# Kernel tuning notes

Hardware: AMD Instinct MI355X
Metric: run time of the kernel (lower is better)

Reference implementation:

```python
import jax, jax.numpy as jnp
import numpy as np

SEQ_LEN = 512
JOINT_DIM = 96
DECAY = 0.8


def _predefined_weights(n: int, decay: float) -> np.ndarray:
    # W[i, j] = decay**(i-j) for j <= i, each row normalized to sum 1.
    i = np.arange(n)[:, None]
    j = np.arange(n)[None, :]
    lower = j <= i
    exponent = np.where(lower, i - j, 0)
    w = np.where(lower, decay ** exponent.astype(np.float64), 0.0)
    row_sum = w.sum(axis=1, keepdims=True)
    w = np.where(row_sum > 0, w / row_sum, w)
    return w.astype(np.float32)


def setup_inputs() -> dict:
    key = jax.random.key(0)
    kx, ko = jax.random.split(key)
    x = jax.random.normal(kx, (64, SEQ_LEN, JOINT_DIM), dtype=jnp.float32)
    # learnable parameter (initialized to zeros in the module; small noise for generality)
    learnable_offset = 0.02 * jax.random.normal(ko, (JOINT_DIM, SEQ_LEN, SEQ_LEN), dtype=jnp.float32)
    predefined_weights = jnp.asarray(_predefined_weights(SEQ_LEN, DECAY))
    return {"x": x, "learnable_offset": learnable_offset, "predefined_weights": predefined_weights}


def reference(x, learnable_offset, predefined_weights):
    # masks[j] = softmax(predefined + offset[j], axis=-1)   -> [J, N, N]
    masks = jax.nn.softmax(predefined_weights[None, :, :] + learnable_offset, axis=-1)
    # out[b, n, j] = sum_m masks[j, n, m] * x[b, m, j]      -> [B, N, J]
    return jnp.einsum('jnm,bmj->bnj', masks, x)
```

## Files before the change

kernel.cpp:

```cpp
#include <hip/hip_runtime.h>

#define BATCH 64
#define SEQ   512
#define JDIM  96
#define TN    64
#define KC    64
#define NCH   (SEQ / KC)
#define LDB   72

typedef __attribute__((ext_vector_type(8))) short bf16x8;
typedef __attribute__((ext_vector_type(4))) float f32x4;

#define LOG2D (-0.32192809489f)

__device__ __forceinline__ unsigned short f2bf(float f) {
  unsigned u = __float_as_uint(f);
  u += 0x7FFFu + ((u >> 16) & 1u);
  return (unsigned short)(u >> 16);
}

__global__ __launch_bounds__(256) void transpose_in_kernel(
    const float* __restrict__ x, unsigned short* __restrict__ xT) {
  __shared__ float tile[JDIM * 65];
  const int r0 = blockIdx.x * 64;
  const int R = BATCH * SEQ;
  for (int idx = threadIdx.x; idx < 64 * 24; idx += 256) {
    int rr = idx / 24, jg = idx - rr * 24;
    float4 v = *(const float4*)(x + (size_t)(r0 + rr) * JDIM + 4 * jg);
    tile[(4 * jg + 0) * 65 + rr] = v.x;
    tile[(4 * jg + 1) * 65 + rr] = v.y;
    tile[(4 * jg + 2) * 65 + rr] = v.z;
    tile[(4 * jg + 3) * 65 + rr] = v.w;
  }
  __syncthreads();
  for (int idx = threadIdx.x; idx < JDIM * 8; idx += 256) {
    int jj = idx >> 3, rg = idx & 7;
    const float* t = &tile[jj * 65 + 8 * rg];
    uint4 pk;
    pk.x = (unsigned)f2bf(t[0]) | ((unsigned)f2bf(t[1]) << 16);
    pk.y = (unsigned)f2bf(t[2]) | ((unsigned)f2bf(t[3]) << 16);
    pk.z = (unsigned)f2bf(t[4]) | ((unsigned)f2bf(t[5]) << 16);
    pk.w = (unsigned)f2bf(t[6]) | ((unsigned)f2bf(t[7]) << 16);
    *(uint4*)(&xT[(size_t)jj * R + r0 + 8 * rg]) = pk;
  }
}

__global__ __launch_bounds__(256, 3) void fused_kernel(
    const unsigned short* __restrict__ xT,
    const float* __restrict__ off,
    float* __restrict__ outT) {
  __shared__ unsigned short As[BATCH * LDB];
  __shared__ unsigned short Bs[TN * LDB];
  __shared__ float Lred[TN * 17];
  __shared__ float Linv[TN];

  const int j  = blockIdx.x >> 3;
  const int n0 = (blockIdx.x & 7) * TN;

  const int tid  = threadIdx.x;
  const int lane = tid & 63;
  const int wid  = tid >> 6;
  const int ln   = lane & 15;
  const int quad = lane >> 4;
  const int bw   = (wid & 1) * 32;
  const int nw   = (wid >> 1) * 32;

  f32x4 acc[2][2];
#pragma unroll
  for (int i = 0; i < 2; ++i)
#pragma unroll
    for (int q = 0; q < 2; ++q) acc[i][q] = (f32x4){0.f, 0.f, 0.f, 0.f};
  float Lpart[4] = {0.f, 0.f, 0.f, 0.f};

  const unsigned short* xTj = xT + (size_t)j * (BATCH * SEQ);
  const float* offj = off + (size_t)j * (SEQ * SEQ);

  const int a_kg = tid & 7;
  const int a_b  = tid >> 3;
  const int b_mg = tid & 15;
  const int b_n  = tid >> 4;

  float cn[4];
#pragma unroll
  for (int p = 0; p < 4; ++p) {
    const int n = n0 + b_n + 16 * p;
    cn[p] = 0.2f / (1.0f - exp2f(LOG2D * (float)(n + 1)));
  }

  for (int ch = 0; ch < NCH; ++ch) {
    const int m0 = ch * KC;
#pragma unroll
    for (int p = 0; p < 2; ++p) {
      const int b = a_b + 32 * p;
      uint4 v = *(const uint4*)(xTj + (size_t)b * SEQ + m0 + 8 * a_kg);
      *(uint4*)(&As[b * LDB + 8 * a_kg]) = v;
    }
    const int mbase = m0 + 4 * b_mg;
#pragma unroll
    for (int p = 0; p < 4; ++p) {
      const int nl = b_n + 16 * p;
      const int n  = n0 + nl;
      const float4 o = *(const float4*)(offj + (size_t)n * SEQ + mbase);
      const float c = cn[p];
      const float d0 = (float)(n - mbase);
      const float p0 = (d0 >= 0.f) ? c * exp2f(LOG2D * d0) : 0.f;
      const float p1 = (d0 >= 1.f) ? c * exp2f(LOG2D * (d0 - 1.f)) : 0.f;
      const float p2 = (d0 >= 2.f) ? c * exp2f(LOG2D * (d0 - 2.f)) : 0.f;
      const float p3 = (d0 >= 3.f) ? c * exp2f(LOG2D * (d0 - 3.f)) : 0.f;
      const float e0 = __expf(o.x + p0);
      const float e1 = __expf(o.y + p1);
      const float e2 = __expf(o.z + p2);
      const float e3 = __expf(o.w + p3);
      Lpart[p] += (e0 + e1) + (e2 + e3);
      uint2 pk;
      pk.x = (unsigned)f2bf(e0) | ((unsigned)f2bf(e1) << 16);
      pk.y = (unsigned)f2bf(e2) | ((unsigned)f2bf(e3) << 16);
      *(uint2*)(&Bs[nl * LDB + 4 * b_mg]) = pk;
    }
    __syncthreads();
#pragma unroll
    for (int ks = 0; ks < KC; ks += 32) {
      bf16x8 afrag[2], bfrag[2];
#pragma unroll
      for (int i = 0; i < 2; ++i)
        afrag[i] = *(const bf16x8*)(&As[(bw + 16 * i + ln) * LDB + ks + 8 * quad]);
#pragma unroll
      for (int q = 0; q < 2; ++q)
        bfrag[q] = *(const bf16x8*)(&Bs[(nw + 16 * q + ln) * LDB + ks + 8 * quad]);
#pragma unroll
      for (int i = 0; i < 2; ++i)
#pragma unroll
        for (int q = 0; q < 2; ++q)
          acc[i][q] = __builtin_amdgcn_mfma_f32_16x16x32_bf16(afrag[i], bfrag[q], acc[i][q], 0, 0, 0);
    }
    __syncthreads();
  }

#pragma unroll
  for (int p = 0; p < 4; ++p) Lred[(b_n + 16 * p) * 17 + b_mg] = Lpart[p];
  __syncthreads();
  if (tid < TN) {
    float s = 0.f;
#pragma unroll
    for (int i = 0; i < 16; ++i) s += Lred[tid * 17 + i];
    Linv[tid] = 1.0f / s;
  }
  __syncthreads();

  float* outTj = outT + (size_t)j * (SEQ * BATCH);
#pragma unroll
  for (int q = 0; q < 2; ++q) {
    const int nc = nw + 16 * q + ln;
    const float linv = Linv[nc];
#pragma unroll
    for (int i = 0; i < 2; ++i) {
      float4 v;
      v.x = acc[i][q][0] * linv;
      v.y = acc[i][q][1] * linv;
      v.z = acc[i][q][2] * linv;
      v.w = acc[i][q][3] * linv;
      *(float4*)(&outTj[(size_t)(n0 + nc) * BATCH + bw + 16 * i + 4 * quad]) = v;
    }
  }
}

__global__ __launch_bounds__(256) void transpose_out_kernel(
    const float* __restrict__ outT, float* __restrict__ out) {
  __shared__ float tile[JDIM * 65];
  const int n = blockIdx.x;
  for (int idx = threadIdx.x; idx < JDIM * 16; idx += 256) {
    int jj = idx >> 4, g = idx & 15;
    float4 v = *(const float4*)(outT + ((size_t)jj * SEQ + n) * BATCH + 4 * g);
    float* t = &tile[jj * 65 + 4 * g];
    t[0] = v.x; t[1] = v.y; t[2] = v.z; t[3] = v.w;
  }
  __syncthreads();
  for (int idx = threadIdx.x; idx < BATCH * 24; idx += 256) {
    int b = idx / 24, jg = idx - b * 24;
    float4 w;
    w.x = tile[(4 * jg + 0) * 65 + b];
    w.y = tile[(4 * jg + 1) * 65 + b];
    w.z = tile[(4 * jg + 2) * 65 + b];
    w.w = tile[(4 * jg + 3) * 65 + b];
    *(float4*)(out + ((size_t)b * SEQ + n) * JDIM + 4 * jg) = w;
  }
}

extern "C" void kernel_launch(void* const* d_in, const int* in_sizes, int n_in,
                              void* d_out, int out_size, void* d_ws, size_t ws_size,
                              hipStream_t stream) {
  const float* x   = (const float*)d_in[0];
  const float* off = (const float*)d_in[1];
  float* out = (float*)d_out;

  unsigned short* xT = (unsigned short*)d_ws;
  float* outT = (float*)((char*)d_ws + (size_t)JDIM * BATCH * SEQ * sizeof(unsigned short));

  transpose_in_kernel<<<BATCH * SEQ / 64, 256, 0, stream>>>(x, xT);
  fused_kernel<<<JDIM * (SEQ / TN), 256, 0, stream>>>(xT, off, outT);
  transpose_out_kernel<<<SEQ, 256, 0, stream>>>(outT, out);
}
```

Measured before the change: 173.7 us.

## Double-buffer fused kernel loads with async global-to-LDS DMA and swizzled layout

Replaces the register-staged global loads of xT and the offset tile with global_load_lds DMA into double-buffered, XOR-swizzled LDS buffers, so the next chunk is prefetched while the current one is processed. The exp computation is reorganised so each thread handles 16 consecutive columns of one row, using a running product (×1.25) instead of per-element exp2, and the bf16 B tile reuses the raw offset buffer in place. This aims to hide global memory latency and cut transcendental work, at the cost of more LDS, extra barriers with manual lgkmcnt waits, and a risk of lower occupancy.

```diff
diff --git a/kernel.cpp b/kernel.cpp
--- a/kernel.cpp
+++ b/kernel.cpp
@@ -7,17 +7,28 @@
 #define KC    64
 #define NCH   (SEQ / KC)
 #define LDB   72
+#define LOG2D (-0.32192809489f)
 
 typedef __attribute__((ext_vector_type(8))) short bf16x8;
 typedef __attribute__((ext_vector_type(4))) float f32x4;
-
-#define LOG2D (-0.32192809489f)
 
 __device__ __forceinline__ unsigned short f2bf(float f) {
   unsigned u = __float_as_uint(f);
   u += 0x7FFFu + ((u >> 16) & 1u);
   return (unsigned short)(u >> 16);
 }
+
+__device__ __forceinline__ void dma16(void* lds, const void* g) {
+  __builtin_amdgcn_global_load_lds(
+      (const __attribute__((address_space(1))) unsigned*)g,
+      (__attribute__((address_space(3))) unsigned*)lds, 16, 0, 0);
+}
+
+#define LGKM_BARRIER() do {                                  \
+  asm volatile("s_waitcnt lgkmcnt(0)" ::: "memory");         \
+  __builtin_amdgcn_s_barrier();                              \
+  asm volatile("" ::: "memory");                             \
+} while (0)
 
 __global__ __launch_bounds__(256) void transpose_in_kernel(
     const float* __restrict__ x, unsigned short* __restrict__ xT) {
@@ -49,9 +60,8 @@
     const unsigned short* __restrict__ xT,
     const float* __restrict__ off,
     float* __restrict__ outT) {
-  __shared__ unsigned short As[BATCH * LDB];
-  __shared__ unsigned short Bs[TN * LDB];
-  __shared__ float Lred[TN * 17];
+  __shared__ __align__(16) unsigned short Araw[2][BATCH * KC];
+  __shared__ __align__(16) float Oraw[2][TN * KC];
   __shared__ float Linv[TN];
 
   const int j  = blockIdx.x >> 3;
@@ -65,84 +75,130 @@
   const int bw   = (wid & 1) * 32;
   const int nw   = (wid >> 1) * 32;
 
-  f32x4 acc[2][2];
-#pragma unroll
-  for (int i = 0; i < 2; ++i)
-#pragma unroll
-    for (int q = 0; q < 2; ++q) acc[i][q] = (f32x4){0.f, 0.f, 0.f, 0.f};
-  float Lpart[4] = {0.f, 0.f, 0.f, 0.f};
-
   const unsigned short* xTj = xT + (size_t)j * (BATCH * SEQ);
   const float* offj = off + (size_t)j * (SEQ * SEQ);
 
-  const int a_kg = tid & 7;
-  const int a_b  = tid >> 3;
-  const int b_mg = tid & 15;
-  const int b_n  = tid >> 4;
-
-  float cn[4];
-#pragma unroll
-  for (int p = 0; p < 4; ++p) {
-    const int n = n0 + b_n + 16 * p;
-    cn[p] = 0.2f / (1.0f - exp2f(LOG2D * (float)(n + 1)));
-  }
+  const unsigned short* pA[2];
+  int aoff[2];
+#pragma unroll
+  for (int t = 0; t < 2; ++t) {
+    const int r = 8 * (2 * wid + t) + (lane >> 3);
+    const int g = (lane & 7) ^ (r & 7);
+    pA[t] = xTj + (size_t)r * SEQ + 8 * g;
+    aoff[t] = (2 * wid + t) * 1024;
+  }
+  const float* pO[4];
+  int ooff[4];
+#pragma unroll
+  for (int t = 0; t < 4; ++t) {
+    const int r = 4 * (4 * wid + t) + (lane >> 4);
+    const int g = (lane & 15) ^ (r & 15);
+    pO[t] = offj + (size_t)(n0 + r) * SEQ + 4 * g;
+    ooff[t] = (4 * wid + t) * 1024;
+  }
+
+#pragma unroll
+  for (int t = 0; t < 2; ++t) dma16((char*)&Araw[0][0] + aoff[t], pA[t]);
+#pragma unroll
+  for (int t = 0; t < 4; ++t) dma16((char*)&Oraw[0][0] + ooff[t], pO[t]);
+
+  f32x4 acc[2][2];
+#pragma unroll
+  for (int i = 0; i < 2; ++i)
+#pragma unroll
+    for (int q = 0; q < 2; ++q) acc[i][q] = (f32x4){0.f, 0.f, 0.f, 0.f};
+
+  const int nl  = tid >> 2;
+  const int sub = tid & 3;
+  const int nglob = n0 + nl;
+  const float cn = 0.2f / (1.0f - exp2f(LOG2D * (float)(nglob + 1)));
+  float Lpart = 0.f;
 
   for (int ch = 0; ch < NCH; ++ch) {
+    const int c = ch & 1;
+    __syncthreads();
+
+    if (ch + 1 < NCH) {
+#pragma unroll
+      for (int t = 0; t < 2; ++t) { pA[t] += KC; dma16((char*)&Araw[c ^ 1][0] + aoff[t], pA[t]); }
+#pragma unroll
+      for (int t = 0; t < 4; ++t) { pO[t] += KC; dma16((char*)&Oraw[c ^ 1][0] + ooff[t], pO[t]); }
+    }
+
+    const char* Ob = (const char*)&Oraw[c][0];
+    float4 o4[4];
+#pragma unroll
+    for (int e = 0; e < 4; ++e) {
+      const int gs = (4 * sub + e) ^ (nl & 15);
+      o4[e] = *(const float4*)(Ob + nl * 256 + gs * 16);
+    }
+    bf16x8 af[2][2];
+#pragma unroll
+    for (int ksI = 0; ksI < 2; ++ksI)
+#pragma unroll
+      for (int i = 0; i < 2; ++i) {
+        const int row = bw + 16 * i + ln;
+        const int gs = ((ksI << 2) + quad) ^ (ln & 7);
+        af[ksI][i] = *(const bf16x8*)((const char*)&Araw[c][0] + row * 128 + gs * 16);
+      }
     const int m0 = ch * KC;
-#pragma unroll
-    for (int p = 0; p < 2; ++p) {
-      const int b = a_b + 32 * p;
-      uint4 v = *(const uint4*)(xTj + (size_t)b * SEQ + m0 + 8 * a_kg);
-      *(uint4*)(&As[b * LDB + 8 * a_kg]) = v;
-    }
-    const int mbase = m0 + 4 * b_mg;
-#pragma unroll
-    for (int p = 0; p < 4; ++p) {
-      const int nl = b_n + 16 * p;
-      const int n  = n0 + nl;
-      const float4 o = *(const float4*)(offj + (size_t)n * SEQ + mbase);
-      const float c = cn[p];
-      const float d0 = (float)(n - mbase);
-      const float p0 = (d0 >= 0.f) ? c * exp2f(LOG2D * d0) : 0.f;
-      const float p1 = (d0 >= 1.f) ? c * exp2f(LOG2D * (d0 - 1.f)) : 0.f;
-      const float p2 = (d0 >= 2.f) ? c * exp2f(LOG2D * (d0 - 2.f)) : 0.f;
-      const float p3 = (d0 >= 3.f) ? c * exp2f(LOG2D * (d0 - 3.f)) : 0.f;
-      const float e0 = __expf(o.x + p0);
-      const float e1 = __expf(o.y + p1);
-      const float e2 = __expf(o.z + p2);
-      const float e3 = __expf(o.w + p3);
-      Lpart[p] += (e0 + e1) + (e2 + e3);
-      uint2 pk;
-      pk.x = (unsigned)f2bf(e0) | ((unsigned)f2bf(e1) << 16);
-      pk.y = (unsigned)f2bf(e2) | ((unsigned)f2bf(e3) << 16);
-      *(uint2*)(&Bs[nl * LDB + 4 * b_mg]) = pk;
-    }
-    __syncthreads();
-#pragma unroll
-    for (int ks = 0; ks < KC; ks += 32) {
-      bf16x8 afrag[2], bfrag[2];
+    const int d0 = nglob - (m0 + 16 * sub);
+    float p = cn * exp2f(LOG2D * (float)(d0 < 0 ? 0 : d0));
+    float ex[16];
+    float ls = 0.f;
+#pragma unroll
+    for (int e = 0; e < 4; ++e) {
+      const float* ov = (const float*)&o4[e];
+#pragma unroll
+      for (int i = 0; i < 4; ++i) {
+        const int q = 4 * e + i;
+        const float pr = (d0 - q >= 0) ? p : 0.f;
+        p *= 1.25f;
+        const float v = __expf(ov[i] + pr);
+        ex[q] = v;
+        ls += v;
+      }
+    }
+    Lpart += ls;
+
+    LGKM_BARRIER();
+
+    unsigned short* Bs = (unsigned short*)&Oraw[c][0];
+    uint4 pk0, pk1;
+    pk0.x = (unsigned)f2bf(ex[0])  | ((unsigned)f2bf(ex[1])  << 16);
+    pk0.y = (unsigned)f2bf(ex[2])  | ((unsigned)f2bf(ex[3])  << 16);
+    pk0.z = (unsigned)f2bf(ex[4])  | ((unsigned)f2bf(ex[5])  << 16);
+    pk0.w = (unsigned)f2bf(ex[6])  | ((unsigned)f2bf(ex[7])  << 16);
+    pk1.x = (unsigned)f2bf(ex[8])  | ((unsigned)f2bf(ex[9])  << 16);
+    pk1.y = (unsigned)f2bf(ex[10]) | ((unsigned)f2bf(ex[11]) << 16);
+    pk1.z = (unsigned)f2bf(ex[12]) | ((unsigned)f2bf(ex[13]) << 16);
+    pk1.w = (unsigned)f2bf(ex[14]) | ((unsigned)f2bf(ex[15]) << 16);
+    *(uint4*)(Bs + nl * LDB + 16 * sub)     = pk0;
+    *(uint4*)(Bs + nl * LDB + 16 * sub + 8) = pk1;
+
+    LGKM_BARRIER();
+
+#pragma unroll
+    for (int ksI = 0; ksI < 2; ++ksI) {
+      bf16x8 bfr[2];
+#pragma unroll
+      for (int q = 0; q < 2; ++q)
+        bfr[q] = *(const bf16x8*)(Bs + (nw + 16 * q + ln) * LDB + 32 * ksI + 8 * quad);
 #pragma unroll
       for (int i = 0; i < 2; ++i)
-        afrag[i] = *(const bf16x8*)(&As[(bw + 16 * i + ln) * LDB + ks + 8 * quad]);
-#pragma unroll
-      for (int q = 0; q < 2; ++q)
-        bfrag[q] = *(const bf16x8*)(&Bs[(nw + 16 * q + ln) * LDB + ks + 8 * quad]);
-#pragma unroll
-      for (int i = 0; i < 2; ++i)
 #pragma unroll
         for (int q = 0; q < 2; ++q)
-          acc[i][q] = __builtin_amdgcn_mfma_f32_16x16x32_bf16(afrag[i], bfrag[q], acc[i][q], 0, 0, 0);
-    }
-    __syncthreads();
-  }
-
-#pragma unroll
-  for (int p = 0; p < 4; ++p) Lred[(b_n + 16 * p) * 17 + b_mg] = Lpart[p];
+          acc[i][q] = __builtin_amdgcn_mfma_f32_16x16x32_bf16(af[ksI][i], bfr[q], acc[i][q], 0, 0, 0);
+    }
+  }
+
+  __syncthreads();
+  float* Lred = (float*)&Araw[0][0];
+  Lred[nl * 5 + sub] = Lpart;
   __syncthreads();
   if (tid < TN) {
-    float s = 0.f;
-#pragma unroll
-    for (int i = 0; i < 16; ++i) s += Lred[tid * 17 + i];
+    const float s = (Lred[tid * 5 + 0] + Lred[tid * 5 + 1]) +
+                    (Lred[tid * 5 + 2] + Lred[tid * 5 + 3]);
     Linv[tid] = 1.0f / s;
   }
   __syncthreads();
```

Result: no change. 175.0 us (+0.7%).
